# Kernel tuning notes

Hardware: AMD Instinct MI355X
Metric: run time of the kernel (lower is better)

Reference implementation:

```python
import jax, jax.numpy as jnp
import numpy as np

N_NODES = 50000
N_EDGES = 800000
IN_DIM = 89
HID = 128


def gcn_conv(x, src, dst, deg_inv_sqrt, W, b):
    # PyG GCNConv: x' = D^{-1/2} (A + I) D^{-1/2} (x W) + b
    h = x @ W  # [N, F_out]
    norm = deg_inv_sqrt[src] * deg_inv_sqrt[dst]  # per-edge norm [E]
    msgs = h[src] * norm[:, None]  # gather + scale [E, F_out]
    agg = jax.ops.segment_sum(msgs, dst, num_segments=x.shape[0])
    # self-loop contribution: norm = deg_inv_sqrt[i]^2
    agg = agg + h * (deg_inv_sqrt * deg_inv_sqrt)[:, None]
    return agg + b


def setup_inputs() -> dict:
    key = jax.random.key(0)
    k1, k2, k3, k4, k5, k6 = jax.random.split(key, 6)
    x = jax.random.normal(k1, (N_NODES, IN_DIM), dtype=jnp.float32)
    edge_index = jax.random.randint(k2, (2, N_EDGES), 0, N_NODES, dtype=jnp.int64)
    # Glorot-style init for GCN weights
    W1 = jax.random.normal(k3, (IN_DIM, HID), dtype=jnp.float32) * (1.0 / np.sqrt(IN_DIM))
    b1 = jnp.zeros((HID,), dtype=jnp.float32)
    W2 = jax.random.normal(k4, (HID, HID), dtype=jnp.float32) * (1.0 / np.sqrt(HID))
    b2 = jnp.zeros((HID,), dtype=jnp.float32)
    return {"x": x, "edge_index": edge_index, "W1": W1, "b1": b1, "W2": W2, "b2": b2}


def reference(x, edge_index, W1, b1, W2, b2):
    src = edge_index[0]
    dst = edge_index[1]
    n = x.shape[0]
    # degree of A + I: 1 (self loop) + in-degree
    deg = 1.0 + jax.ops.segment_sum(jnp.ones((src.shape[0],), x.dtype), dst, num_segments=n)
    deg_inv_sqrt = jax.lax.rsqrt(deg)
    h = jax.nn.relu(gcn_conv(x, src, dst, deg_inv_sqrt, W1, b1))
    h = jax.nn.relu(gcn_conv(h, src, dst, deg_inv_sqrt, W2, b2))
    return (h, edge_index)
```

## Files before the change

### kernel.cpp

```cpp
#include <hip/hip_runtime.h>
#include <hip/hip_bf16.h>


#define HID 128
#define KIN 89
#define KP 96
#define BSH 8
#define BNODES 256
#define MAXBUCK 256
#define NPB 128
#define P4CAP 6144

typedef __attribute__((ext_vector_type(8))) short bf16x8;
typedef __attribute__((ext_vector_type(4))) float f32x4;

static __device__ inline float2 unpack_bf16(unsigned v) {
    union { unsigned u; float f; } lo, hi;
    lo.u = v << 16;
    hi.u = v & 0xFFFF0000u;
    return make_float2(lo.f, hi.f);
}

static __device__ inline unsigned pack_bf16(float a, float b) {
    __hip_bfloat162 h = __float22bfloat162_rn(make_float2(a, b));
    return *reinterpret_cast<unsigned*>(&h);
}

static __device__ inline unsigned short f2bf(float v) {
    __hip_bfloat16 h = __float2bfloat16(v);
    return *reinterpret_cast<unsigned short*>(&h);
}


__global__ __launch_bounds__(256) void prep_kernel(
    const int* __restrict__ ei, float* __restrict__ outE,
    const float* __restrict__ X, unsigned* __restrict__ Xh,
    const float* __restrict__ W1, unsigned short* __restrict__ W1t,
    const float* __restrict__ W2, unsigned short* __restrict__ W2t,
    int N, int E)
{
    const int nA = 2 * E;
    const int nB = N * (KP / 2);
    const int nC = HID * KP;
    const int nD = HID * HID;
    int i = blockIdx.x * 256 + threadIdx.x;
    if (i < nA) {
        outE[i] = (float)ei[i];
        return;
    }
    i -= nA;
    if (i < nB) {
        int n = i / (KP / 2);
        int c = i % (KP / 2);
        const float* xr = X + (size_t)n * KIN;
        float a = (2 * c     < KIN) ? xr[2 * c]     : 0.0f;
        float b = (2 * c + 1 < KIN) ? xr[2 * c + 1] : 0.0f;
        Xh[(size_t)n * (KP / 2) + c] = pack_bf16(a, b);
        return;
    }
    i -= nB;
    if (i < nC) {
        int n = i / KP, k = i % KP;
        float v = (k < KIN) ? W1[(size_t)k * HID + n] : 0.0f;
        W1t[i] = f2bf(v);
        return;
    }
    i -= nC;
    if (i < nD) {
        int n = i / HID, k = i % HID;
        W2t[i] = f2bf(W2[(size_t)k * HID + n]);
    }
}


__global__ __launch_bounds__(256) void p1_hist_kernel(
    const int* __restrict__ dst, int* __restrict__ histG, int E, int nbuck)
{
    __shared__ int h[MAXBUCK];
    const int tid = threadIdx.x, blk = blockIdx.x;
    const int chunk = (E + NPB - 1) / NPB;
    const int beg = blk * chunk, end = min(beg + chunk, E);
    if (tid < nbuck) h[tid] = 0;
    __syncthreads();
    for (int i = beg + tid; i < end; i += 256)
        atomicAdd(&h[dst[i] >> BSH], 1);
    __syncthreads();
    if (tid < nbuck) histG[tid * NPB + blk] = h[tid];
}

__global__ __launch_bounds__(NPB) void p2a_kernel(
    int* __restrict__ histG, int* __restrict__ totals)
{
    __shared__ int wsum[NPB / 64];
    const int b = blockIdx.x, tid = threadIdx.x, lane = tid & 63, wid = tid >> 6;
    int c = histG[b * NPB + tid];
    int s = c;
#pragma unroll
    for (int off = 1; off < 64; off <<= 1) {
        int t = __shfl_up(s, off, 64);
        if (lane >= off) s += t;
    }
    if (lane == 63) wsum[wid] = s;
    __syncthreads();
    if (tid == 0) {
        int a = 0;
#pragma unroll
        for (int w = 0; w < NPB / 64; ++w) { int t = wsum[w]; wsum[w] = a; a += t; }
    }
    __syncthreads();
    int excl = wsum[wid] + s - c;
    histG[b * NPB + tid] = excl;
    if (tid == NPB - 1) totals[b] = excl + c;
}

static __device__ inline void scan_totals(const int* __restrict__ totals,
                                          int* __restrict__ sexcl,
                                          int* __restrict__ wsum,
                                          int nbuck, int tid)
{
    const int lane = tid & 63, wid = tid >> 6;
    int v = (tid < nbuck) ? totals[tid] : 0;
    int s = v;
#pragma unroll
    for (int off = 1; off < 64; off <<= 1) {
        int t = __shfl_up(s, off, 64);
        if (lane >= off) s += t;
    }
    if (lane == 63) wsum[wid] = s;
    __syncthreads();
    if (tid == 0) {
        int a = 0;
#pragma unroll
        for (int w = 0; w < 4; ++w) { int t = wsum[w]; wsum[w] = a; a += t; }
    }
    __syncthreads();
    sexcl[tid] = wsum[wid] + s - v;
}

__global__ __launch_bounds__(256) void p3_part_kernel(
    const int* __restrict__ src, const int* __restrict__ dst,
    const int* __restrict__ histG, const int* __restrict__ totals,
    unsigned* __restrict__ ebuf, int E, int nbuck)
{
    __shared__ int cur[MAXBUCK];
    __shared__ int wsum[4];
    const int tid = threadIdx.x, blk = blockIdx.x;
    scan_totals(totals, cur, wsum, nbuck, tid);
    __syncthreads();
    if (tid < nbuck) cur[tid] += histG[tid * NPB + blk];
    const int chunk = (E + NPB - 1) / NPB;
    const int beg = blk * chunk, end = min(beg + chunk, E);
    __syncthreads();
    for (int i = beg + tid; i < end; i += 256) {
        int d = dst[i];
        int b = d >> BSH;
        int pos = atomicAdd(&cur[b], 1);
        ebuf[pos] = ((unsigned)(d & (BNODES - 1)) << 16) | (unsigned)src[i];
    }
}

__global__ __launch_bounds__(256) void p4_sort_kernel(
    const unsigned* __restrict__ ebuf, const int* __restrict__ totals,
    unsigned short* __restrict__ csr, int* __restrict__ rowptr,
    float* __restrict__ dis, int N, int E, int nbuck)
{
    __shared__ int counts[BNODES];
    __shared__ int cursor[BNODES];
    __shared__ int sbase[MAXBUCK];
    __shared__ int wsum[4];
    __shared__ unsigned short staging[P4CAP];
    const int b = blockIdx.x, tid = threadIdx.x, lane = tid & 63, wid = tid >> 6;

    scan_totals(totals, sbase, wsum, nbuck, tid);
    __syncthreads();
    const int gbase = sbase[b];
    const int cnt = totals[b];

    counts[tid] = 0;
    __syncthreads();
    for (int i = tid; i < cnt; i += 256)
        atomicAdd(&counts[ebuf[gbase + i] >> 16], 1);
    __syncthreads();

    int c = counts[tid];
    int s = c;
#pragma unroll
    for (int off = 1; off < 64; off <<= 1) {
        int t = __shfl_up(s, off, 64);
        if (lane >= off) s += t;
    }
    if (lane == 63) wsum[wid] = s;
    __syncthreads();
    if (tid == 0) {
        int a = 0;
#pragma unroll
        for (int w = 0; w < 4; ++w) { int t = wsum[w]; wsum[w] = a; a += t; }
    }
    __syncthreads();
    int excl = wsum[wid] + s - c;
    cursor[tid] = excl;
    int node = b * BNODES + tid;
    if (node < N) {
        rowptr[node] = gbase + excl;
        dis[node] = rsqrtf(1.0f + (float)c);
    }
    if (b == 0 && tid == 0) rowptr[N] = E;
    __syncthreads();

    if (cnt <= P4CAP) {
        for (int i = tid; i < cnt; i += 256) {
            unsigned v = ebuf[gbase + i];
            int pos = atomicAdd(&cursor[v >> 16], 1);
            staging[pos] = (unsigned short)(v & 0xFFFFu);
        }
        __syncthreads();
        for (int i = tid; i < cnt; i += 256)
            csr[gbase + i] = staging[i];
    } else {
        for (int i = tid; i < cnt; i += 256) {
            unsigned v = ebuf[gbase + i];
            int pos = atomicAdd(&cursor[v >> 16], 1);
            csr[gbase + pos] = (unsigned short)(v & 0xFFFFu);
        }
    }
}


__global__ __launch_bounds__(256) void gather_x_kernel(
    const unsigned* __restrict__ Xh, const int* __restrict__ rowptr,
    const unsigned short* __restrict__ csr, const float* __restrict__ dis,
    unsigned* __restrict__ aggh, int N)
{
    int node = blockIdx.x * 4 + (threadIdx.x >> 6);
    if (node >= N) return;
    int lane = threadIdx.x & 63;
    bool act = lane < (KP / 2);
    float di = dis[node];

    float a0 = 0.0f, a1 = 0.0f;
    if (act) {
        float2 v = unpack_bf16(Xh[(size_t)node * (KP / 2) + lane]);
        a0 = di * v.x; a1 = di * v.y;
    }

    int beg = rowptr[node], end = rowptr[node + 1];
    int j = beg;
    for (; j + 4 <= end; j += 4) {
        int s0 = csr[j], s1 = csr[j + 1], s2 = csr[j + 2], s3 = csr[j + 3];
        float d0 = dis[s0], d1 = dis[s1], d2 = dis[s2], d3 = dis[s3];
        if (act) {
            float2 v0 = unpack_bf16(Xh[(size_t)s0 * (KP / 2) + lane]);
            float2 v1 = unpack_bf16(Xh[(size_t)s1 * (KP / 2) + lane]);
            float2 v2 = unpack_bf16(Xh[(size_t)s2 * (KP / 2) + lane]);
            float2 v3 = unpack_bf16(Xh[(size_t)s3 * (KP / 2) + lane]);
            a0 += d0 * v0.x + d1 * v1.x + d2 * v2.x + d3 * v3.x;
            a1 += d0 * v0.y + d1 * v1.y + d2 * v2.y + d3 * v3.y;
        }
    }
    for (; j < end; ++j) {
        int s = csr[j];
        float d = dis[s];
        if (act) {
            float2 v = unpack_bf16(Xh[(size_t)s * (KP / 2) + lane]);
            a0 += d * v.x; a1 += d * v.y;
        }
    }
    if (act)
        aggh[(size_t)node * (KP / 2) + lane] = pack_bf16(di * a0, di * a1);
}

__global__ __launch_bounds__(256) void gather_h_kernel(
    const unsigned* __restrict__ g, const int* __restrict__ rowptr,
    const unsigned short* __restrict__ csr, const float* __restrict__ dis,
    unsigned* __restrict__ aggh, int N)
{
    int node = blockIdx.x * 4 + (threadIdx.x >> 6);
    if (node >= N) return;
    int lane = threadIdx.x & 63;
    int beg = rowptr[node], end = rowptr[node + 1];

    float2 sv = unpack_bf16(g[(size_t)node * (HID / 2) + lane]);
    float a0 = sv.x, a1 = sv.y;
    int j = beg;
    for (; j + 4 <= end; j += 4) {
        int s0 = csr[j], s1 = csr[j + 1], s2 = csr[j + 2], s3 = csr[j + 3];
        float2 v0 = unpack_bf16(g[(size_t)s0 * (HID / 2) + lane]);
        float2 v1 = unpack_bf16(g[(size_t)s1 * (HID / 2) + lane]);
        float2 v2 = unpack_bf16(g[(size_t)s2 * (HID / 2) + lane]);
        float2 v3 = unpack_bf16(g[(size_t)s3 * (HID / 2) + lane]);
        a0 += v0.x + v1.x + v2.x + v3.x;
        a1 += v0.y + v1.y + v2.y + v3.y;
    }
    for (; j < end; ++j) {
        int s = csr[j];
        float2 v = unpack_bf16(g[(size_t)s * (HID / 2) + lane]);
        a0 += v.x; a1 += v.y;
    }
    float di = dis[node];
    aggh[(size_t)node * (HID / 2) + lane] = pack_bf16(a0 * di, a1 * di);
}

template<int KPA, bool LAYER1>
__global__ __launch_bounds__(256) void mfma_gemm_kernel(
    const unsigned short* __restrict__ A, const unsigned short* __restrict__ Wt,
    const float* __restrict__ bias, const float* __restrict__ dis,
    void* __restrict__ outp, int N)
{
    const int wave = threadIdx.x >> 6;
    const int lane = threadIdx.x & 63;
    const int m    = lane & 15;
    const int quad = lane >> 4;
    const int row0 = blockIdx.x * 64 + wave * 16;
    const int node = row0 + m;

    f32x4 acc[8];
#pragma unroll
    for (int t = 0; t < 8; ++t) acc[t] = (f32x4){0.0f, 0.0f, 0.0f, 0.0f};

    const int arow = min(node, N - 1);
    const unsigned short* arp = A + (size_t)arow * KPA;

#pragma unroll
    for (int c = 0; c < KPA / 32; ++c) {
        const int k0 = c * 32 + quad * 8;
        bf16x8 nv = *(const bf16x8*)(arp + k0);
#pragma unroll
        for (int t = 0; t < 8; ++t) {
            bf16x8 wv = *(const bf16x8*)(Wt + (size_t)(t * 16 + m) * KPA + k0);
            acc[t] = __builtin_amdgcn_mfma_f32_16x16x32_bf16(wv, nv, acc[t], 0, 0, 0);
        }
    }

    if (node < N) {
        const float dv = LAYER1 ? dis[node] : 1.0f;
#pragma unroll
        for (int t = 0; t < 8; ++t) {
            const int col0 = t * 16 + quad * 4;
            float4 bb = *(const float4*)&bias[col0];
            float r0 = fmaxf(acc[t][0] + bb.x, 0.0f);
            float r1 = fmaxf(acc[t][1] + bb.y, 0.0f);
            float r2 = fmaxf(acc[t][2] + bb.z, 0.0f);
            float r3 = fmaxf(acc[t][3] + bb.w, 0.0f);
            if (LAYER1) {
                uint2 u;
                u.x = pack_bf16(r0 * dv, r1 * dv);
                u.y = pack_bf16(r2 * dv, r3 * dv);
                *(uint2*)((unsigned short*)outp + (size_t)node * HID + col0) = u;
            } else {
                float4 r = make_float4(r0, r1, r2, r3);
                *(float4*)((float*)outp + (size_t)node * HID + col0) = r;
            }
        }
    }
}


static inline char* wsal(char*& p, size_t n) {
    uintptr_t q = ((uintptr_t)p + 255) & ~(uintptr_t)255;
    char* r = (char*)q;
    p = r + n;
    return r;
}

extern "C" void kernel_launch(void* const* d_in, const int* in_sizes, int n_in,
                              void* d_out, int out_size, void* d_ws, size_t ws_size,
                              hipStream_t stream) {
    const float* x  = (const float*)d_in[0];
    const int*   ei = (const int*)d_in[1];
    const float* W1 = (const float*)d_in[2];
    const float* b1 = (const float*)d_in[3];
    const float* W2 = (const float*)d_in[4];
    const float* b2 = (const float*)d_in[5];

    const int N = in_sizes[0] / KIN;
    const int E = in_sizes[1] / 2;
    const int* src = ei;
    const int* dst = ei + E;
    const int nbuck = (N + BNODES - 1) >> BSH;

    float* out  = (float*)d_out;
    float* outH = out;
    float* outE = out + (size_t)N * HID;

    char* ws = (char*)d_ws;
    int*            histG  = (int*)wsal(ws, (size_t)MAXBUCK * NPB * 4);
    int*            totals = (int*)wsal(ws, MAXBUCK * 4);
    int*            rowptr = (int*)wsal(ws, (size_t)(N + 1) * 4);
    float*          dis    = (float*)wsal(ws, (size_t)N * 4);
    unsigned*       ebuf   = (unsigned*)wsal(ws, (size_t)E * 4);
    unsigned short* csr    = (unsigned short*)wsal(ws, (size_t)E * 2);
    unsigned*       Xh     = (unsigned*)wsal(ws, (size_t)N * (KP / 2) * 4);
    unsigned*       agg1h  = (unsigned*)wsal(ws, (size_t)N * (KP / 2) * 4);
    unsigned short* g2h    = (unsigned short*)wsal(ws, (size_t)N * HID * 2);
    unsigned short* agg2h  = (unsigned short*)wsal(ws, (size_t)N * HID * 2);
    unsigned short* W1t    = (unsigned short*)wsal(ws, (size_t)HID * KP * 2);
    unsigned short* W2t    = (unsigned short*)wsal(ws, (size_t)HID * HID * 2);

    {
        const int total = 2 * E + N * (KP / 2) + HID * KP + HID * HID;
        prep_kernel<<<(total + 255) / 256, 256, 0, stream>>>(
            ei, outE, x, Xh, W1, W1t, W2, W2t, N, E);
    }

    p1_hist_kernel<<<NPB, 256, 0, stream>>>(dst, histG, E, nbuck);
    p2a_kernel<<<nbuck, NPB, 0, stream>>>(histG, totals);
    p3_part_kernel<<<NPB, 256, 0, stream>>>(src, dst, histG, totals, ebuf, E, nbuck);
    p4_sort_kernel<<<nbuck, 256, 0, stream>>>(ebuf, totals, csr, rowptr, dis, N, E, nbuck);

    const int ngt = (N + 3) / 4;
    const int ngm = (N + 63) / 64;

    gather_x_kernel<<<ngt, 256, 0, stream>>>(Xh, rowptr, csr, dis, agg1h, N);
    mfma_gemm_kernel<KP, true><<<ngm, 256, 0, stream>>>(
        (const unsigned short*)agg1h, W1t, b1, dis, g2h, N);

    gather_h_kernel<<<ngt, 256, 0, stream>>>((const unsigned*)g2h, rowptr, csr, dis,
                                             (unsigned*)agg2h, N);
    mfma_gemm_kernel<HID, false><<<ngm, 256, 0, stream>>>(
        agg2h, W2t, b2, dis, outH, N);
}
```

Before: 236.0 us.

## Fuse neighbor gather with MFMA GEMM per layer and fold prep into partition kernels

Merges each layer's CSR gather and the following bf16 MFMA GEMM into one kernel. Aggregated rows are staged in LDS instead of round-tripping through global memory. The prep kernel is removed: the edge-index float copy and weight transposes move into the histogram kernel, and the pre-scaled bf16 X conversion moves into the sort kernel. Neighbor indices are loaded once per wave and broadcast with shuffles, and scaling by the destination's inverse sqrt degree is applied in the GEMM epilogue. This cuts two launches and the intermediate traffic, but the fused kernels launch only N/64 blocks, each wave gathers 16 nodes serially, and occupancy or latency hiding may suffer.

```diff
diff --git a/kernel.cpp b/kernel.cpp
--- a/kernel.cpp
+++ b/kernel.cpp
@@ -31,59 +31,40 @@
     return *reinterpret_cast<unsigned short*>(&h);
 }
 
-
-__global__ __launch_bounds__(256) void prep_kernel(
+__global__ __launch_bounds__(256) void p1_kernel(
     const int* __restrict__ ei, float* __restrict__ outE,
-    const float* __restrict__ X, unsigned* __restrict__ Xh,
+    int* __restrict__ histG,
     const float* __restrict__ W1, unsigned short* __restrict__ W1t,
     const float* __restrict__ W2, unsigned short* __restrict__ W2t,
-    int N, int E)
-{
-    const int nA = 2 * E;
-    const int nB = N * (KP / 2);
-    const int nC = HID * KP;
-    const int nD = HID * HID;
-    int i = blockIdx.x * 256 + threadIdx.x;
-    if (i < nA) {
-        outE[i] = (float)ei[i];
-        return;
-    }
-    i -= nA;
-    if (i < nB) {
-        int n = i / (KP / 2);
-        int c = i % (KP / 2);
-        const float* xr = X + (size_t)n * KIN;
-        float a = (2 * c     < KIN) ? xr[2 * c]     : 0.0f;
-        float b = (2 * c + 1 < KIN) ? xr[2 * c + 1] : 0.0f;
-        Xh[(size_t)n * (KP / 2) + c] = pack_bf16(a, b);
-        return;
-    }
-    i -= nB;
-    if (i < nC) {
-        int n = i / KP, k = i % KP;
-        float v = (k < KIN) ? W1[(size_t)k * HID + n] : 0.0f;
-        W1t[i] = f2bf(v);
-        return;
-    }
-    i -= nC;
-    if (i < nD) {
-        int n = i / HID, k = i % HID;
-        W2t[i] = f2bf(W2[(size_t)k * HID + n]);
-    }
-}
-
-
-__global__ __launch_bounds__(256) void p1_hist_kernel(
-    const int* __restrict__ dst, int* __restrict__ histG, int E, int nbuck)
+    int E, int nbuck)
 {
     __shared__ int h[MAXBUCK];
     const int tid = threadIdx.x, blk = blockIdx.x;
+    const int* src = ei;
+    const int* dst = ei + E;
+    if (tid < nbuck) h[tid] = 0;
+
+    int tg = blk * 256 + tid;
+    if (tg < HID * KP) {
+        int n = tg / KP, k = tg % KP;
+        W1t[tg] = f2bf(k < KIN ? W1[(size_t)k * HID + n] : 0.0f);
+    } else {
+        int t2 = tg - HID * KP;
+        if (t2 < HID * HID) {
+            int n = t2 / HID, k = t2 % HID;
+            W2t[t2] = f2bf(W2[(size_t)k * HID + n]);
+        }
+    }
+    __syncthreads();
+
     const int chunk = (E + NPB - 1) / NPB;
     const int beg = blk * chunk, end = min(beg + chunk, E);
-    if (tid < nbuck) h[tid] = 0;
-    __syncthreads();
-    for (int i = beg + tid; i < end; i += 256)
-        atomicAdd(&h[dst[i] >> BSH], 1);
+    for (int i = beg + tid; i < end; i += 256) {
+        int d = dst[i];
+        atomicAdd(&h[d >> BSH], 1);
+        outE[i] = (float)src[i];
+        outE[E + i] = (float)d;
+    }
     __syncthreads();
     if (tid < nbuck) histG[tid * NPB + blk] = h[tid];
 }
@@ -138,13 +119,15 @@
 }
 
 __global__ __launch_bounds__(256) void p3_part_kernel(
-    const int* __restrict__ src, const int* __restrict__ dst,
-    const int* __restrict__ histG, const int* __restrict__ totals,
-    unsigned* __restrict__ ebuf, int E, int nbuck)
+    const int* __restrict__ ei, const int* __restrict__ histG,
+    const int* __restrict__ totals, unsigned* __restrict__ ebuf,
+    int E, int nbuck)
 {
     __shared__ int cur[MAXBUCK];
     __shared__ int wsum[4];
     const int tid = threadIdx.x, blk = blockIdx.x;
+    const int* src = ei;
+    const int* dst = ei + E;
     scan_totals(totals, cur, wsum, nbuck, tid);
     __syncthreads();
     if (tid < nbuck) cur[tid] += histG[tid * NPB + blk];
@@ -162,12 +145,14 @@
 __global__ __launch_bounds__(256) void p4_sort_kernel(
     const unsigned* __restrict__ ebuf, const int* __restrict__ totals,
     unsigned short* __restrict__ csr, int* __restrict__ rowptr,
-    float* __restrict__ dis, int N, int E, int nbuck)
+    float* __restrict__ dis, const float* __restrict__ X,
+    unsigned* __restrict__ Xhs, int N, int E, int nbuck)
 {
     __shared__ int counts[BNODES];
     __shared__ int cursor[BNODES];
     __shared__ int sbase[MAXBUCK];
     __shared__ int wsum[4];
+    __shared__ float sdis[BNODES];
     __shared__ unsigned short staging[P4CAP];
     const int b = blockIdx.x, tid = threadIdx.x, lane = tid & 63, wid = tid >> 6;
 
@@ -199,10 +184,12 @@
     __syncthreads();
     int excl = wsum[wid] + s - c;
     cursor[tid] = excl;
+    float dd = rsqrtf(1.0f + (float)c);
+    sdis[tid] = dd;
     int node = b * BNODES + tid;
     if (node < N) {
         rowptr[node] = gbase + excl;
-        dis[node] = rsqrtf(1.0f + (float)c);
+        dis[node] = dd;
     }
     if (b == 0 && tid == 0) rowptr[N] = E;
     __syncthreads();
@@ -223,107 +210,90 @@
             csr[gbase + pos] = (unsigned short)(v & 0xFFFFu);
         }
     }
-}
-
-
-__global__ __launch_bounds__(256) void gather_x_kernel(
-    const unsigned* __restrict__ Xh, const int* __restrict__ rowptr,
+
+    const int nodeBase = b * BNODES;
+    for (int idx = tid; idx < BNODES * (KP / 2); idx += 256) {
+        int nl = idx / (KP / 2), cc = idx % (KP / 2);
+        int nd = nodeBase + nl;
+        if (nd < N) {
+            const float* xr = X + (size_t)nd * KIN;
+            float d = sdis[nl];
+            float a = (2 * cc     < KIN) ? d * xr[2 * cc]     : 0.0f;
+            float bb = (2 * cc + 1 < KIN) ? d * xr[2 * cc + 1] : 0.0f;
+            Xhs[(size_t)nd * (KP / 2) + cc] = pack_bf16(a, bb);
+        }
+    }
+}
+
+template<int KPA, bool LAYER1>
+__global__ __launch_bounds__(256) void fused_layer_kernel(
+    const unsigned* __restrict__ rows, const int* __restrict__ rowptr,
     const unsigned short* __restrict__ csr, const float* __restrict__ dis,
-    unsigned* __restrict__ aggh, int N)
-{
-    int node = blockIdx.x * 4 + (threadIdx.x >> 6);
-    if (node >= N) return;
-    int lane = threadIdx.x & 63;
-    bool act = lane < (KP / 2);
-    float di = dis[node];
-
-    float a0 = 0.0f, a1 = 0.0f;
-    if (act) {
-        float2 v = unpack_bf16(Xh[(size_t)node * (KP / 2) + lane]);
-        a0 = di * v.x; a1 = di * v.y;
-    }
-
-    int beg = rowptr[node], end = rowptr[node + 1];
-    int j = beg;
-    for (; j + 4 <= end; j += 4) {
-        int s0 = csr[j], s1 = csr[j + 1], s2 = csr[j + 2], s3 = csr[j + 3];
-        float d0 = dis[s0], d1 = dis[s1], d2 = dis[s2], d3 = dis[s3];
-        if (act) {
-            float2 v0 = unpack_bf16(Xh[(size_t)s0 * (KP / 2) + lane]);
-            float2 v1 = unpack_bf16(Xh[(size_t)s1 * (KP / 2) + lane]);
-            float2 v2 = unpack_bf16(Xh[(size_t)s2 * (KP / 2) + lane]);
-            float2 v3 = unpack_bf16(Xh[(size_t)s3 * (KP / 2) + lane]);
-            a0 += d0 * v0.x + d1 * v1.x + d2 * v2.x + d3 * v3.x;
-            a1 += d0 * v0.y + d1 * v1.y + d2 * v2.y + d3 * v3.y;
-        }
-    }
-    for (; j < end; ++j) {
-        int s = csr[j];
-        float d = dis[s];
-        if (act) {
-            float2 v = unpack_bf16(Xh[(size_t)s * (KP / 2) + lane]);
-            a0 += d * v.x; a1 += d * v.y;
-        }
-    }
-    if (act)
-        aggh[(size_t)node * (KP / 2) + lane] = pack_bf16(di * a0, di * a1);
-}
-
-__global__ __launch_bounds__(256) void gather_h_kernel(
-    const unsigned* __restrict__ g, const int* __restrict__ rowptr,
-    const unsigned short* __restrict__ csr, const float* __restrict__ dis,
-    unsigned* __restrict__ aggh, int N)
-{
-    int node = blockIdx.x * 4 + (threadIdx.x >> 6);
-    if (node >= N) return;
-    int lane = threadIdx.x & 63;
-    int beg = rowptr[node], end = rowptr[node + 1];
-
-    float2 sv = unpack_bf16(g[(size_t)node * (HID / 2) + lane]);
-    float a0 = sv.x, a1 = sv.y;
-    int j = beg;
-    for (; j + 4 <= end; j += 4) {
-        int s0 = csr[j], s1 = csr[j + 1], s2 = csr[j + 2], s3 = csr[j + 3];
-        float2 v0 = unpack_bf16(g[(size_t)s0 * (HID / 2) + lane]);
-        float2 v1 = unpack_bf16(g[(size_t)s1 * (HID / 2) + lane]);
-        float2 v2 = unpack_bf16(g[(size_t)s2 * (HID / 2) + lane]);
-        float2 v3 = unpack_bf16(g[(size_t)s3 * (HID / 2) + lane]);
-        a0 += v0.x + v1.x + v2.x + v3.x;
-        a1 += v0.y + v1.y + v2.y + v3.y;
-    }
-    for (; j < end; ++j) {
-        int s = csr[j];
-        float2 v = unpack_bf16(g[(size_t)s * (HID / 2) + lane]);
-        a0 += v.x; a1 += v.y;
-    }
-    float di = dis[node];
-    aggh[(size_t)node * (HID / 2) + lane] = pack_bf16(a0 * di, a1 * di);
-}
-
-template<int KPA, bool LAYER1>
-__global__ __launch_bounds__(256) void mfma_gemm_kernel(
-    const unsigned short* __restrict__ A, const unsigned short* __restrict__ Wt,
-    const float* __restrict__ bias, const float* __restrict__ dis,
+    const unsigned short* __restrict__ Wt, const float* __restrict__ bias,
     void* __restrict__ outp, int N)
 {
+    constexpr int PAIRS = KPA / 2;
+    constexpr int S = PAIRS + 4;
+    __shared__ unsigned lds[64 * S];
     const int wave = threadIdx.x >> 6;
     const int lane = threadIdx.x & 63;
+    const int node0 = blockIdx.x * 64;
+    const bool act = lane < PAIRS;
+
+    for (int i = 0; i < 16; ++i) {
+        const int nl = wave * 16 + i;
+        const int node = node0 + nl;
+        float a0 = 0.0f, a1 = 0.0f;
+        if (node < N) {
+            if (act) {
+                float2 v = unpack_bf16(rows[(size_t)node * PAIRS + lane]);
+                a0 = v.x; a1 = v.y;
+            }
+            const int beg = rowptr[node], end = rowptr[node + 1];
+            for (int cb = beg; cb < end; cb += 64) {
+                const int cnt = min(64, end - cb);
+                int idxv = csr[cb + (lane < cnt ? lane : cnt - 1)];
+                int j = 0;
+                for (; j + 4 <= cnt; j += 4) {
+                    int s0 = __shfl(idxv, j);
+                    int s1 = __shfl(idxv, j + 1);
+                    int s2 = __shfl(idxv, j + 2);
+                    int s3 = __shfl(idxv, j + 3);
+                    if (act) {
+                        float2 v0 = unpack_bf16(rows[(size_t)s0 * PAIRS + lane]);
+                        float2 v1 = unpack_bf16(rows[(size_t)s1 * PAIRS + lane]);
+                        float2 v2 = unpack_bf16(rows[(size_t)s2 * PAIRS + lane]);
+                        float2 v3 = unpack_bf16(rows[(size_t)s3 * PAIRS + lane]);
+                        a0 += v0.x + v1.x + v2.x + v3.x;
+                        a1 += v0.y + v1.y + v2.y + v3.y;
+                    }
+                }
+                for (; j < cnt; ++j) {
+                    int sx = __shfl(idxv, j);
+                    if (act) {
+                        float2 v = unpack_bf16(rows[(size_t)sx * PAIRS + lane]);
+                        a0 += v.x; a1 += v.y;
+                    }
+                }
+            }
+        }
+        if (act) lds[nl * S + lane] = pack_bf16(a0, a1);
+    }
+    __syncthreads();
+
     const int m    = lane & 15;
     const int quad = lane >> 4;
-    const int row0 = blockIdx.x * 64 + wave * 16;
-    const int node = row0 + m;
+    const int nl   = wave * 16 + m;
+    const int node = node0 + nl;
 
     f32x4 acc[8];
 #pragma unroll
     for (int t = 0; t < 8; ++t) acc[t] = (f32x4){0.0f, 0.0f, 0.0f, 0.0f};
 
-    const int arow = min(node, N - 1);
-    const unsigned short* arp = A + (size_t)arow * KPA;
-
 #pragma unroll
     for (int c = 0; c < KPA / 32; ++c) {
+        bf16x8 nv = *(const bf16x8*)(lds + nl * S + c * 16 + quad * 4);
         const int k0 = c * 32 + quad * 8;
-        bf16x8 nv = *(const bf16x8*)(arp + k0);
 #pragma unroll
         for (int t = 0; t < 8; ++t) {
             bf16x8 wv = *(const bf16x8*)(Wt + (size_t)(t * 16 + m) * KPA + k0);
@@ -332,15 +302,15 @@
     }
 
     if (node < N) {
-        const float dv = LAYER1 ? dis[node] : 1.0f;
+        const float dv = dis[node];
 #pragma unroll
         for (int t = 0; t < 8; ++t) {
             const int col0 = t * 16 + quad * 4;
             float4 bb = *(const float4*)&bias[col0];
-            float r0 = fmaxf(acc[t][0] + bb.x, 0.0f);
-            float r1 = fmaxf(acc[t][1] + bb.y, 0.0f);
-            float r2 = fmaxf(acc[t][2] + bb.z, 0.0f);
-            float r3 = fmaxf(acc[t][3] + bb.w, 0.0f);
+            float r0 = fmaxf(fmaf(dv, acc[t][0], bb.x), 0.0f);
+            float r1 = fmaxf(fmaf(dv, acc[t][1], bb.y), 0.0f);
+            float r2 = fmaxf(fmaf(dv, acc[t][2], bb.z), 0.0f);
+            float r3 = fmaxf(fmaf(dv, acc[t][3], bb.w), 0.0f);
             if (LAYER1) {
                 uint2 u;
                 u.x = pack_bf16(r0 * dv, r1 * dv);
@@ -374,8 +344,6 @@
 
     const int N = in_sizes[0] / KIN;
     const int E = in_sizes[1] / 2;
-    const int* src = ei;
-    const int* dst = ei + E;
     const int nbuck = (N + BNODES - 1) >> BSH;
 
     float* out  = (float*)d_out;
@@ -389,33 +357,20 @@
     float*          dis    = (float*)wsal(ws, (size_t)N * 4);
     unsigned*       ebuf   = (unsigned*)wsal(ws, (size_t)E * 4);
     unsigned short* csr    = (unsigned short*)wsal(ws, (size_t)E * 2);
-    unsigned*       Xh     = (unsigned*)wsal(ws, (size_t)N * (KP / 2) * 4);
-    unsigned*       agg1h  = (unsigned*)wsal(ws, (size_t)N * (KP / 2) * 4);
+    unsigned*       Xhs    = (unsigned*)wsal(ws, (size_t)N * (KP / 2) * 4);
     unsigned short* g2h    = (unsigned short*)wsal(ws, (size_t)N * HID * 2);
-    unsigned short* agg2h  = (unsigned short*)wsal(ws, (size_t)N * HID * 2);
     unsigned short* W1t    = (unsigned short*)wsal(ws, (size_t)HID * KP * 2);
     unsigned short* W2t    = (unsigned short*)wsal(ws, (size_t)HID * HID * 2);
 
-    {
-        const int total = 2 * E + N * (KP / 2) + HID * KP + HID * HID;
-        prep_kernel<<<(total + 255) / 256, 256, 0, stream>>>(
-            ei, outE, x, Xh, W1, W1t, W2, W2t, N, E);
-    }
-
-    p1_hist_kernel<<<NPB, 256, 0, stream>>>(dst, histG, E, nbuck);
+    p1_kernel<<<NPB, 256, 0, stream>>>(ei, outE, histG, W1, W1t, W2, W2t, E, nbuck);
     p2a_kernel<<<nbuck, NPB, 0, stream>>>(histG, totals);
-    p3_part_kernel<<<NPB, 256, 0, stream>>>(src, dst, histG, totals, ebuf, E, nbuck);
-    p4_sort_kernel<<<nbuck, 256, 0, stream>>>(ebuf, totals, csr, rowptr, dis, N, E, nbuck);
-
-    const int ngt = (N + 3) / 4;
+    p3_part_kernel<<<NPB, 256, 0, stream>>>(ei, histG, totals, ebuf, E, nbuck);
+    p4_sort_kernel<<<nbuck, 256, 0, stream>>>(ebuf, totals, csr, rowptr, dis,
+                                              x, Xhs, N, E, nbuck);
+
     const int ngm = (N + 63) / 64;
-
-    gather_x_kernel<<<ngt, 256, 0, stream>>>(Xh, rowptr, csr, dis, agg1h, N);
-    mfma_gemm_kernel<KP, true><<<ngm, 256, 0, stream>>>(
-        (const unsigned short*)agg1h, W1t, b1, dis, g2h, N);
-
-    gather_h_kernel<<<ngt, 256, 0, stream>>>((const unsigned*)g2h, rowptr, csr, dis,
-                                             (unsigned*)agg2h, N);
-    mfma_gemm_kernel<HID, false><<<ngm, 256, 0, stream>>>(
-        agg2h, W2t, b2, dis, outH, N);
-}
+    fused_layer_kernel<KP, true><<<ngm, 256, 0, stream>>>(
+        Xhs, rowptr, csr, dis, W1t, b1, g2h, N);
+    fused_layer_kernel<HID, false><<<ngm, 256, 0, stream>>>(
+        (const unsigned*)g2h, rowptr, csr, dis, W2t, b2, outH, N);
+}
```

Measured after the change: 268.4 us. 13.7% more time.
